# Performance work log

Measured on AMD Instinct MI355X. Metric: run time of the kernel, lower is better.

Reference implementation:

```python
import jax, jax.numpy as jnp
import numpy as np

B, C, H, W = 2, 64, 270, 480
CQ = C // 8


def _distance_weight(n):
    i = jnp.arange(n, dtype=jnp.float32)
    d = i[None, :] - i[:, None]  # j - i
    return jnp.exp(-(d * d) / (2.0 * (n * n / 4.0)))  # [n, n]


def setup_inputs() -> dict:
    key = jax.random.key(0)
    ks = jax.random.split(key, 8)
    s = 0.05
    return {
        "x": jax.random.normal(ks[0], (B, C, H, W), jnp.float32),
        "Wq": jax.random.normal(ks[1], (CQ, C), jnp.float32) * s,
        "bq": jax.random.normal(ks[2], (CQ,), jnp.float32) * s,
        "Wk": jax.random.normal(ks[3], (CQ, C), jnp.float32) * s,
        "bk": jax.random.normal(ks[4], (CQ,), jnp.float32) * s,
        "Wv": jax.random.normal(ks[5], (C, C), jnp.float32) * s,
        "bv": jax.random.normal(ks[6], (C,), jnp.float32) * s,
        "gamma": jax.random.normal(ks[7], (), jnp.float32) * 0.3,
        "dw_h": _distance_weight(H),  # [H, H] non-trainable buffer
        "dw_w": _distance_weight(W),  # [W, W] non-trainable buffer
    }


def reference(x, Wq, bq, Wk, bk, Wv, bv, gamma, dw_h, dw_w):
    # 1x1 convs == per-pixel linear projections
    q = jnp.einsum('oc,bchw->bohw', Wq, x) + bq[None, :, None, None]  # [B,CQ,H,W]
    k = jnp.einsum('oc,bchw->bohw', Wk, x) + bk[None, :, None, None]  # [B,CQ,H,W]
    v = jnp.einsum('oc,bchw->bohw', Wv, x) + bv[None, :, None, None]  # [B,C,H,W]

    height, width = x.shape[2], x.shape[3]
    neg_inf = jnp.float32(-jnp.inf)

    # row (H-direction) energy: queries/keys along the height axis per column w
    e_h = jnp.einsum('bchw,bcgw->bwhg', q, k) * dw_h[None, None]  # [B,W,H,H]
    # diagonal -inf mask (dw_h diag == 1, so order of mul is immaterial)
    eye_h = jnp.eye(height, dtype=bool)
    e_h = jnp.where(eye_h[None, None], neg_inf, e_h)
    e_h = jnp.transpose(e_h, (0, 2, 1, 3))  # [B,H,W,H]

    # column (W-direction) energy along the width axis per row h
    e_w = jnp.einsum('bchw,bchv->bhwv', q, k) * dw_w[None, None]  # [B,H,W,W]

    # joint softmax over concatenated H and W directions
    att = jax.nn.softmax(jnp.concatenate([e_h, e_w], axis=3), axis=3)  # [B,H,W,H+W]
    att_h = jnp.transpose(att[:, :, :, :height], (0, 2, 1, 3))  # [B,W,H,H]
    att_w = att[:, :, :, height:]  # [B,H,W,W]

    out_h = jnp.einsum('bcgw,bwhg->bchw', v, att_h)  # [B,C,H,W]
    out_w = jnp.einsum('bchv,bhwv->bchw', v, att_w)  # [B,C,H,W]

    return gamma * (out_h + out_w) + x
```

## Files before the change

### kernel.cpp

```cpp
#include <hip/hip_runtime.h>
#include <hip/hip_bf16.h>

namespace {

constexpr int B  = 2;
constexpr int C  = 64;
constexpr int CQ = 8;
constexpr int H  = 270;
constexpr int W  = 480;
constexpr int HW = H * W;
constexpr float INVH2 = 2.0f / (270.0f * 270.0f);
constexpr float INVW2 = 2.0f / (480.0f * 480.0f);

typedef __attribute__((ext_vector_type(4))) float f32x4;
typedef __attribute__((ext_vector_type(8))) short short8;
typedef __attribute__((ext_vector_type(4))) unsigned int uint4v;

__device__ __forceinline__ float bits2f(unsigned short u) {
  union { unsigned int i; float f; } cv;
  cv.i = ((unsigned int)u) << 16;
  return cv.f;
}

__device__ __forceinline__ unsigned short f2bf(float f) {
  union { __hip_bfloat16 b; unsigned short u; } cv;
  cv.b = __float2bfloat16(f);
  return cv.u;
}

__device__ __forceinline__ unsigned int pack2(float a, float b) {
  return ((unsigned int)f2bf(b) << 16) | (unsigned int)f2bf(a);
}

__device__ __forceinline__ short8 pack_p(const float p0[4], const float p1[4]) {
  uint4v pw;
  pw[0] = pack2(p0[0], p0[1]);
  pw[1] = pack2(p0[2], p0[3]);
  pw[2] = pack2(p1[0], p1[1]);
  pw[3] = pack2(p1[2], p1[3]);
  return __builtin_bit_cast(short8, pw);
}


__global__ __launch_bounds__(256)
void k_qkv(const float* __restrict__ x,
           const float* __restrict__ Wq, const float* __restrict__ bq,
           const float* __restrict__ Wk, const float* __restrict__ bk,
           const float* __restrict__ Wv, const float* __restrict__ bv,
           unsigned short* __restrict__ qwp, unsigned short* __restrict__ kwp,
           unsigned short* __restrict__ qhp, unsigned short* __restrict__ khp,
           unsigned short* __restrict__ v, unsigned short* __restrict__ vt) {
  __shared__ __align__(16) float wql[CQ * C];
  __shared__ __align__(16) float wkl[CQ * C];
  __shared__ __align__(16) float wvl[C * C];
  __shared__ float bql[CQ], bkl[CQ], bvl[C];
  const int tid = threadIdx.x;
  for (int i = tid; i < CQ * C; i += 256) { wql[i] = Wq[i]; wkl[i] = Wk[i]; }
  for (int i = tid; i < C * C; i += 256) wvl[i] = Wv[i];
  if (tid < CQ) { bql[tid] = bq[tid]; bkl[tid] = bk[tid]; }
  if (tid < C) bvl[tid] = bv[tid];
  __syncthreads();
  const int pix = blockIdx.x * 256 + tid;
  if (pix >= B * HW) return;
  const int b = pix / HW;
  const int r = pix - b * HW;
  const int h = r / W;
  const int w = r - h * W;

  float qa[CQ], ka[CQ], va[C];
#pragma unroll
  for (int o = 0; o < CQ; ++o) { qa[o] = bql[o]; ka[o] = bkl[o]; }
#pragma unroll
  for (int o = 0; o < C; ++o) va[o] = bvl[o];

  const float* xp = x + (size_t)b * C * HW + r;
  for (int c = 0; c < C; c += 4) {
    const float x0 = xp[(size_t)(c + 0) * HW];
    const float x1 = xp[(size_t)(c + 1) * HW];
    const float x2 = xp[(size_t)(c + 2) * HW];
    const float x3 = xp[(size_t)(c + 3) * HW];
#pragma unroll
    for (int o = 0; o < CQ; ++o) {
      const float4 a = *(const float4*)(wql + o * C + c);
      qa[o] = fmaf(a.w, x3, fmaf(a.z, x2, fmaf(a.y, x1, fmaf(a.x, x0, qa[o]))));
      const float4 bb = *(const float4*)(wkl + o * C + c);
      ka[o] = fmaf(bb.w, x3, fmaf(bb.z, x2, fmaf(bb.y, x1, fmaf(bb.x, x0, ka[o]))));
    }
#pragma unroll
    for (int o = 0; o < C; ++o) {
      const float4 cc = *(const float4*)(wvl + o * C + c);
      va[o] = fmaf(cc.w, x3, fmaf(cc.z, x2, fmaf(cc.y, x1, fmaf(cc.x, x0, va[o]))));
    }
  }

  uint4 qp4, kp4;
  qp4.x = pack2(qa[0], qa[1]); qp4.y = pack2(qa[2], qa[3]);
  qp4.z = pack2(qa[4], qa[5]); qp4.w = pack2(qa[6], qa[7]);
  kp4.x = pack2(ka[0], ka[1]); kp4.y = pack2(ka[2], ka[3]);
  kp4.z = pack2(ka[4], ka[5]); kp4.w = pack2(ka[6], ka[7]);
  *(uint4*)(qwp + (size_t)pix * 8) = qp4;
  *(uint4*)(kwp + (size_t)pix * 8) = kp4;
  const size_t tbase = ((size_t)b * W + w) * H + h;
  *(uint4*)(qhp + tbase * 8) = qp4;
  *(uint4*)(khp + tbase * 8) = kp4;

  unsigned short* vp = v + (size_t)b * C * HW + r;
#pragma unroll
  for (int o = 0; o < C; ++o) vp[(size_t)o * HW] = f2bf(va[o]);
  unsigned short* vtp = vt + tbase * C;
#pragma unroll
  for (int j = 0; j < 16; ++j) {
    ushort4 u;
    u.x = f2bf(va[4 * j + 0]);
    u.y = f2bf(va[4 * j + 1]);
    u.z = f2bf(va[4 * j + 2]);
    u.w = f2bf(va[4 * j + 3]);
    *(ushort4*)(vtp + 4 * j) = u;
  }
}

constexpr int VSW = 488;

__global__ __launch_bounds__(960, 1)
void k_outw(const unsigned short* __restrict__ qwp,
            const unsigned short* __restrict__ kwp,
            const unsigned short* __restrict__ v,
            unsigned short* __restrict__ ow, float* __restrict__ Sw) {
  __shared__ __align__(16) unsigned short vbs[31232];
  __shared__ __align__(16) unsigned short kls[480 * 8];
  const int h = blockIdx.x, b = blockIdx.y;
  const int tid = threadIdx.x;
  const size_t rowbase = ((size_t)b * H + h) * W;

  const unsigned short* vrow = v + (size_t)b * C * HW + (size_t)h * W;
  for (int idx = tid; idx < 64 * 120; idx += 960) {
    const int c = idx / 120, s4 = (idx - c * 120) * 4;
    const int u = s4 & 31;
    const int t = (u < 16) ? ((u >> 2) * 8) : (((u - 16) >> 2) * 8 + 4);
    *(ushort4*)(vbs + c * VSW + (s4 & ~31) + t) =
        *(const ushort4*)(vrow + (size_t)c * HW + s4);
  }
  for (int g = tid; g < 480; g += 960)
    *(uint4*)(kls + g * 8) = *(const uint4*)(kwp + (rowbase + g) * 8);

  const int lane = tid & 63, wv = tid >> 6;
  const int l15 = lane & 15, quad = lane >> 4;
  const int m0 = wv * 32;

  short8 qa0 = short8{0, 0, 0, 0, 0, 0, 0, 0};
  short8 qa1 = short8{0, 0, 0, 0, 0, 0, 0, 0};
  if (quad == 0) {
    qa0 = *(const short8*)(qwp + (rowbase + m0 + l15) * 8);
    qa1 = *(const short8*)(qwp + (rowbase + m0 + 16 + l15) * 8);
  }

  f32x4 acc[2][4];
  float Sacc[2] = {0.0f, 0.0f};
#pragma unroll
  for (int mt = 0; mt < 2; ++mt)
#pragma unroll
    for (int ct = 0; ct < 4; ++ct)
#pragma unroll
      for (int rr = 0; rr < 4; ++rr) acc[mt][ct][rr] = 0.0f;

  __syncthreads();

  for (int ci = 0; ci < 15; ++ci) {
    const int sc = ci * 32;
    short8 kb0 = short8{0, 0, 0, 0, 0, 0, 0, 0};
    short8 kb1 = short8{0, 0, 0, 0, 0, 0, 0, 0};
    if (quad == 0) {
      kb0 = *(const short8*)(kls + (sc + l15) * 8);
      kb1 = *(const short8*)(kls + (sc + 16 + l15) * 8);
    }
    const f32x4 z4 = f32x4{0.f, 0.f, 0.f, 0.f};
    const f32x4 E00 = __builtin_amdgcn_mfma_f32_16x16x32_bf16(kb0, qa0, z4, 0, 0, 0);
    const f32x4 E01 = __builtin_amdgcn_mfma_f32_16x16x32_bf16(kb1, qa0, z4, 0, 0, 0);
    const f32x4 E10 = __builtin_amdgcn_mfma_f32_16x16x32_bf16(kb0, qa1, z4, 0, 0, 0);
    const f32x4 E11 = __builtin_amdgcn_mfma_f32_16x16x32_bf16(kb1, qa1, z4, 0, 0, 0);
    short8 vb[4];
#pragma unroll
    for (int ct = 0; ct < 4; ++ct)
      vb[ct] = *(const short8*)(vbs + (ct * 16 + l15) * VSW + sc + quad * 8);
#pragma unroll
    for (int mt = 0; mt < 2; ++mt) {
      const int m = m0 + mt * 16 + l15;
      const f32x4 Ea = mt ? E10 : E00;
      const f32x4 Eb = mt ? E11 : E01;
      float p0[4], p1[4];
#pragma unroll
      for (int rr = 0; rr < 4; ++rr) {
        const float d0 = (float)(m - (sc + quad * 4 + rr));
        const float d1 = d0 - 16.0f;
        p0[rr] = __expf(Ea[rr] * __expf(-(d0 * d0) * INVW2));
        p1[rr] = __expf(Eb[rr] * __expf(-(d1 * d1) * INVW2));
        Sacc[mt] += p0[rr] + p1[rr];
      }
      const short8 pa = pack_p(p0, p1);
#pragma unroll
      for (int ct = 0; ct < 4; ++ct)
        acc[mt][ct] = __builtin_amdgcn_mfma_f32_16x16x32_bf16(pa, vb[ct], acc[mt][ct], 0, 0, 0);
    }
  }

#pragma unroll
  for (int mt = 0; mt < 2; ++mt) {
    float s = Sacc[mt];
    s += __shfl_xor(s, 16);
    s += __shfl_xor(s, 32);
    if (lane < 16) Sw[rowbase + m0 + mt * 16 + l15] = s;
  }

  __syncthreads();
  unsigned short* ob = vbs;
#pragma unroll
  for (int mt = 0; mt < 2; ++mt)
#pragma unroll
    for (int ct = 0; ct < 4; ++ct)
#pragma unroll
      for (int rr = 0; rr < 4; ++rr)
        ob[(ct * 16 + l15) * VSW + m0 + mt * 16 + quad * 4 + rr] = f2bf(acc[mt][ct][rr]);
  __syncthreads();
  unsigned short* og = ow + ((size_t)b * H + h) * C * W;
  for (int idx = tid; idx < 64 * 240; idx += 960) {
    const int c = idx / 240, wp = idx - c * 240;
    *(unsigned int*)(og + (size_t)c * W + 2 * wp) =
        *(const unsigned int*)(ob + c * VSW + 2 * wp);
  }
}

constexpr int VSH = 296;

__global__ __launch_bounds__(576, 1)
void k_outh(const unsigned short* __restrict__ qhp,
            const unsigned short* __restrict__ khp,
            const unsigned short* __restrict__ vt,
            unsigned short* __restrict__ oht, float* __restrict__ Sht) {
  __shared__ __align__(16) unsigned short vbs[18944];
  __shared__ __align__(16) unsigned short kls[288 * 8];
  const int w = blockIdx.x, b = blockIdx.y;
  const int tid = threadIdx.x;
  const size_t colbase = ((size_t)b * W + w) * H;

  const unsigned short* vtb = vt + ((size_t)b * W + w) * H * C;
  for (int idx = tid; idx < 288 * 16; idx += 576) {
    const int g = idx >> 4, c4 = (idx & 15) * 4;
    ushort4 vv = make_ushort4(0, 0, 0, 0);
    if (g < H) vv = *(const ushort4*)(vtb + (size_t)g * C + c4);
    const int u = g & 31;
    const int t = (u < 16) ? ((u >> 2) * 8 + (u & 3))
                           : (((u - 16) >> 2) * 8 + 4 + (u & 3));
    const int slot = (g & ~31) + t;
    vbs[(c4 + 0) * VSH + slot] = vv.x;
    vbs[(c4 + 1) * VSH + slot] = vv.y;
    vbs[(c4 + 2) * VSH + slot] = vv.z;
    vbs[(c4 + 3) * VSH + slot] = vv.w;
  }
  for (int g = tid; g < 288; g += 576)
    *(uint4*)(kls + g * 8) =
        *(const uint4*)(khp + (colbase + min(g, H - 1)) * 8);

  const int lane = tid & 63, wv = tid >> 6;
  const int l15 = lane & 15, quad = lane >> 4;
  const int m0 = wv * 32;

  short8 qa0 = short8{0, 0, 0, 0, 0, 0, 0, 0};
  short8 qa1 = short8{0, 0, 0, 0, 0, 0, 0, 0};
  if (quad == 0) {
    qa0 = *(const short8*)(qhp + (colbase + min(m0 + l15, H - 1)) * 8);
    qa1 = *(const short8*)(qhp + (colbase + min(m0 + 16 + l15, H - 1)) * 8);
  }

  f32x4 acc[2][4];
  float Sacc[2] = {0.0f, 0.0f};
#pragma unroll
  for (int mt = 0; mt < 2; ++mt)
#pragma unroll
    for (int ct = 0; ct < 4; ++ct)
#pragma unroll
      for (int rr = 0; rr < 4; ++rr) acc[mt][ct][rr] = 0.0f;

  __syncthreads();

  for (int ci = 0; ci < 9; ++ci) {
    const int gc = ci * 32;
    short8 kb0 = short8{0, 0, 0, 0, 0, 0, 0, 0};
    short8 kb1 = short8{0, 0, 0, 0, 0, 0, 0, 0};
    if (quad == 0) {
      kb0 = *(const short8*)(kls + (gc + l15) * 8);
      kb1 = *(const short8*)(kls + (gc + 16 + l15) * 8);
    }
    const f32x4 z4 = f32x4{0.f, 0.f, 0.f, 0.f};
    const f32x4 E00 = __builtin_amdgcn_mfma_f32_16x16x32_bf16(kb0, qa0, z4, 0, 0, 0);
    const f32x4 E01 = __builtin_amdgcn_mfma_f32_16x16x32_bf16(kb1, qa0, z4, 0, 0, 0);
    const f32x4 E10 = __builtin_amdgcn_mfma_f32_16x16x32_bf16(kb0, qa1, z4, 0, 0, 0);
    const f32x4 E11 = __builtin_amdgcn_mfma_f32_16x16x32_bf16(kb1, qa1, z4, 0, 0, 0);
    short8 vb[4];
#pragma unroll
    for (int ct = 0; ct < 4; ++ct)
      vb[ct] = *(const short8*)(vbs + (ct * 16 + l15) * VSH + gc + quad * 8);
#pragma unroll
    for (int mt = 0; mt < 2; ++mt) {
      const int m = m0 + mt * 16 + l15;
      const f32x4 Ea = mt ? E10 : E00;
      const f32x4 Eb = mt ? E11 : E01;
      float p0[4], p1[4];
#pragma unroll
      for (int rr = 0; rr < 4; ++rr) {
        const int g0 = gc + quad * 4 + rr;
        const int g1 = g0 + 16;
        const float d0 = (float)(m - g0);
        const float d1 = d0 - 16.0f;
        p0[rr] = (g0 < H && g0 != m)
                     ? __expf(Ea[rr] * __expf(-(d0 * d0) * INVH2)) : 0.0f;
        p1[rr] = (g1 < H && g1 != m)
                     ? __expf(Eb[rr] * __expf(-(d1 * d1) * INVH2)) : 0.0f;
        Sacc[mt] += p0[rr] + p1[rr];
      }
      const short8 pa = pack_p(p0, p1);
#pragma unroll
      for (int ct = 0; ct < 4; ++ct)
        acc[mt][ct] = __builtin_amdgcn_mfma_f32_16x16x32_bf16(pa, vb[ct], acc[mt][ct], 0, 0, 0);
    }
  }

#pragma unroll
  for (int mt = 0; mt < 2; ++mt) {
    float s = Sacc[mt];
    s += __shfl_xor(s, 16);
    s += __shfl_xor(s, 32);
    const int m = m0 + mt * 16 + l15;
    if (lane < 16 && m < H) Sht[colbase + m] = s;
  }

  __syncthreads();
  unsigned short* ob = vbs;
#pragma unroll
  for (int mt = 0; mt < 2; ++mt)
#pragma unroll
    for (int ct = 0; ct < 4; ++ct)
#pragma unroll
      for (int rr = 0; rr < 4; ++rr)
        ob[(ct * 16 + l15) * VSH + m0 + mt * 16 + quad * 4 + rr] = f2bf(acc[mt][ct][rr]);
  __syncthreads();
  unsigned short* og = oht + ((size_t)b * W + w) * C * H;
  for (int idx = tid; idx < 64 * 135; idx += 576) {
    const int c = idx / 135, hp = idx - c * 135;
    *(unsigned int*)(og + (size_t)c * H + 2 * hp) =
        *(const unsigned int*)(ob + c * VSH + 2 * hp);
  }
}

__global__ __launch_bounds__(256)
void k_combine(const unsigned short* __restrict__ oht,
               const unsigned short* __restrict__ ow,
               const float* __restrict__ Sht, const float* __restrict__ Sw,
               const float* __restrict__ x,
               const float* __restrict__ gp,
               float* __restrict__ out) {
  __shared__ float tile[32][33];
  const int b = blockIdx.z >> 6, c = blockIdx.z & 63;
  const int w0 = blockIdx.x * 32, h0 = blockIdx.y * 32;
  const int tx = threadIdx.x, ty = threadIdx.y;
#pragma unroll
  for (int i = 0; i < 4; ++i) {
    const int wl = ty + i * 8;
    const int hh = h0 + tx;
    float val = 0.0f;
    if (hh < H) val = bits2f(oht[(((size_t)b * W + (w0 + wl)) * C + c) * H + hh]);
    tile[wl][tx] = val;
  }
  __syncthreads();
  const float gamma = *gp;
#pragma unroll
  for (int i = 0; i < 4; ++i) {
    const int hl = ty + i * 8;
    const int hh = h0 + hl;
    if (hh < H) {
      const int ww = w0 + tx;
      const float uh = tile[tx][hl];
      const float uw = bits2f(ow[(((size_t)b * H + hh) * C + c) * W + ww]);
      const size_t si = ((size_t)b * H + hh) * W + ww;
      const float Z = Sht[((size_t)b * W + ww) * H + hh] + Sw[si];
      const float invZ = __builtin_amdgcn_rcpf(Z);
      const size_t xi = ((size_t)b * C + c) * HW + (size_t)hh * W + ww;
      out[xi] = fmaf(gamma * invZ, uh + uw, x[xi]);
    }
  }
}

}

extern "C" void kernel_launch(void* const* d_in, const int* in_sizes, int n_in,
                              void* d_out, int out_size, void* d_ws, size_t ws_size,
                              hipStream_t stream) {
  (void)in_sizes; (void)n_in; (void)out_size; (void)ws_size;
  const float* x  = (const float*)d_in[0];
  const float* Wq = (const float*)d_in[1];
  const float* bq = (const float*)d_in[2];
  const float* Wk = (const float*)d_in[3];
  const float* bk = (const float*)d_in[4];
  const float* Wv = (const float*)d_in[5];
  const float* bv = (const float*)d_in[6];
  const float* gp = (const float*)d_in[7];
  float* out = (float*)d_out;

  char* p = (char*)d_ws;
  auto take = [&](size_t bytes) -> void* {
    char* r = p;
    p += (bytes + 255) & ~(size_t)255;
    return (void*)r;
  };
  unsigned short* qwp = (unsigned short*)take(sizeof(unsigned short) * (size_t)B * HW * 8);
  unsigned short* kwp = (unsigned short*)take(sizeof(unsigned short) * (size_t)B * HW * 8);
  unsigned short* qhp = (unsigned short*)take(sizeof(unsigned short) * (size_t)B * HW * 8);
  unsigned short* khp = (unsigned short*)take(sizeof(unsigned short) * (size_t)B * HW * 8);
  unsigned short* v   = (unsigned short*)take(sizeof(unsigned short) * (size_t)B * C * HW);
  unsigned short* vt  = (unsigned short*)take(sizeof(unsigned short) * (size_t)B * C * HW);
  unsigned short* oht = (unsigned short*)take(sizeof(unsigned short) * (size_t)B * C * HW);
  unsigned short* owb = (unsigned short*)take(sizeof(unsigned short) * (size_t)B * C * HW);
  float* Sht = (float*)take(sizeof(float) * (size_t)B * HW);
  float* Sw  = (float*)take(sizeof(float) * (size_t)B * HW);

  hipLaunchKernelGGL(k_qkv, dim3((B * HW + 255) / 256), dim3(256), 0, stream,
                     x, Wq, bq, Wk, bk, Wv, bv, qwp, kwp, qhp, khp, v, vt);
  hipLaunchKernelGGL(k_outh, dim3(W, B), dim3(576), 0, stream,
                     qhp, khp, vt, oht, Sht);
  hipLaunchKernelGGL(k_outw, dim3(H, B), dim3(960), 0, stream,
                     qwp, kwp, v, owb, Sw);
  hipLaunchKernelGGL(k_combine, dim3(W / 32, (H + 31) / 32, B * C), dim3(32, 8), 0, stream,
                     oht, owb, Sht, Sw, x, gp, out);
}
```

Measured before the change: 454.1 us.

## Split row and column attention blocks in two along the query axis

Each k_outw and k_outh block now handles only half of the query chunks, with twice as many smaller blocks (512 and 320 threads). Both halves still stage the full V row or column and K into LDS, and each writes back only its own part of the output. The LDS row strides are also padded differently (494 and 302). The aim is better load balance and more blocks per CU, which may help latency hiding. The cost is that the V/K staging loads are duplicated, and some waves sit idle because 15 and 9 chunks do not split evenly.

```diff
diff --git a/kernel.cpp b/kernel.cpp
--- a/kernel.cpp
+++ b/kernel.cpp
@@ -119,37 +119,40 @@
   }
 }
 
-constexpr int VSW = 488;
-
-__global__ __launch_bounds__(960, 1)
+constexpr int VSW = 494;
+
+__global__ __launch_bounds__(512, 1)
 void k_outw(const unsigned short* __restrict__ qwp,
             const unsigned short* __restrict__ kwp,
             const unsigned short* __restrict__ v,
             unsigned short* __restrict__ ow, float* __restrict__ Sw) {
-  __shared__ __align__(16) unsigned short vbs[31232];
+  __shared__ __align__(16) unsigned short vbs[64 * VSW];
   __shared__ __align__(16) unsigned short kls[480 * 8];
-  const int h = blockIdx.x, b = blockIdx.y;
+  const int h = blockIdx.x >> 1, z = blockIdx.x & 1;
+  const int b = blockIdx.y;
   const int tid = threadIdx.x;
   const size_t rowbase = ((size_t)b * H + h) * W;
 
   const unsigned short* vrow = v + (size_t)b * C * HW + (size_t)h * W;
-  for (int idx = tid; idx < 64 * 120; idx += 960) {
+  for (int idx = tid; idx < 64 * 120; idx += 512) {
     const int c = idx / 120, s4 = (idx - c * 120) * 4;
     const int u = s4 & 31;
     const int t = (u < 16) ? ((u >> 2) * 8) : (((u - 16) >> 2) * 8 + 4);
     *(ushort4*)(vbs + c * VSW + (s4 & ~31) + t) =
         *(const ushort4*)(vrow + (size_t)c * HW + s4);
   }
-  for (int g = tid; g < 480; g += 960)
+  for (int g = tid; g < 480; g += 512)
     *(uint4*)(kls + g * 8) = *(const uint4*)(kwp + (rowbase + g) * 8);
 
   const int lane = tid & 63, wv = tid >> 6;
   const int l15 = lane & 15, quad = lane >> 4;
-  const int m0 = wv * 32;
+  const int chunk = z * 8 + wv;
+  const bool active = chunk < 15;
+  const int m0 = chunk * 32;
 
   short8 qa0 = short8{0, 0, 0, 0, 0, 0, 0, 0};
   short8 qa1 = short8{0, 0, 0, 0, 0, 0, 0, 0};
-  if (quad == 0) {
+  if (quad == 0 && active) {
     qa0 = *(const short8*)(qwp + (rowbase + m0 + l15) * 8);
     qa1 = *(const short8*)(qwp + (rowbase + m0 + 16 + l15) * 8);
   }
@@ -165,85 +168,92 @@
 
   __syncthreads();
 
-  for (int ci = 0; ci < 15; ++ci) {
-    const int sc = ci * 32;
-    short8 kb0 = short8{0, 0, 0, 0, 0, 0, 0, 0};
-    short8 kb1 = short8{0, 0, 0, 0, 0, 0, 0, 0};
-    if (quad == 0) {
-      kb0 = *(const short8*)(kls + (sc + l15) * 8);
-      kb1 = *(const short8*)(kls + (sc + 16 + l15) * 8);
-    }
-    const f32x4 z4 = f32x4{0.f, 0.f, 0.f, 0.f};
-    const f32x4 E00 = __builtin_amdgcn_mfma_f32_16x16x32_bf16(kb0, qa0, z4, 0, 0, 0);
-    const f32x4 E01 = __builtin_amdgcn_mfma_f32_16x16x32_bf16(kb1, qa0, z4, 0, 0, 0);
-    const f32x4 E10 = __builtin_amdgcn_mfma_f32_16x16x32_bf16(kb0, qa1, z4, 0, 0, 0);
-    const f32x4 E11 = __builtin_amdgcn_mfma_f32_16x16x32_bf16(kb1, qa1, z4, 0, 0, 0);
-    short8 vb[4];
-#pragma unroll
-    for (int ct = 0; ct < 4; ++ct)
-      vb[ct] = *(const short8*)(vbs + (ct * 16 + l15) * VSW + sc + quad * 8);
+  if (active) {
+    for (int ci = 0; ci < 15; ++ci) {
+      const int sc = ci * 32;
+      short8 kb0 = short8{0, 0, 0, 0, 0, 0, 0, 0};
+      short8 kb1 = short8{0, 0, 0, 0, 0, 0, 0, 0};
+      if (quad == 0) {
+        kb0 = *(const short8*)(kls + (sc + l15) * 8);
+        kb1 = *(const short8*)(kls + (sc + 16 + l15) * 8);
+      }
+      const f32x4 z4 = f32x4{0.f, 0.f, 0.f, 0.f};
+      const f32x4 E00 = __builtin_amdgcn_mfma_f32_16x16x32_bf16(kb0, qa0, z4, 0, 0, 0);
+      const f32x4 E01 = __builtin_amdgcn_mfma_f32_16x16x32_bf16(kb1, qa0, z4, 0, 0, 0);
+      const f32x4 E10 = __builtin_amdgcn_mfma_f32_16x16x32_bf16(kb0, qa1, z4, 0, 0, 0);
+      const f32x4 E11 = __builtin_amdgcn_mfma_f32_16x16x32_bf16(kb1, qa1, z4, 0, 0, 0);
+      short8 vb[4];
+#pragma unroll
+      for (int ct = 0; ct < 4; ++ct)
+        vb[ct] = *(const short8*)(vbs + (ct * 16 + l15) * VSW + sc + quad * 8);
+#pragma unroll
+      for (int mt = 0; mt < 2; ++mt) {
+        const int m = m0 + mt * 16 + l15;
+        const f32x4 Ea = mt ? E10 : E00;
+        const f32x4 Eb = mt ? E11 : E01;
+        float p0[4], p1[4];
+#pragma unroll
+        for (int rr = 0; rr < 4; ++rr) {
+          const float d0 = (float)(m - (sc + quad * 4 + rr));
+          const float d1 = d0 - 16.0f;
+          p0[rr] = __expf(Ea[rr] * __expf(-(d0 * d0) * INVW2));
+          p1[rr] = __expf(Eb[rr] * __expf(-(d1 * d1) * INVW2));
+          Sacc[mt] += p0[rr] + p1[rr];
+        }
+        const short8 pa = pack_p(p0, p1);
+#pragma unroll
+        for (int ct = 0; ct < 4; ++ct)
+          acc[mt][ct] = __builtin_amdgcn_mfma_f32_16x16x32_bf16(pa, vb[ct], acc[mt][ct], 0, 0, 0);
+      }
+    }
+
 #pragma unroll
     for (int mt = 0; mt < 2; ++mt) {
-      const int m = m0 + mt * 16 + l15;
-      const f32x4 Ea = mt ? E10 : E00;
-      const f32x4 Eb = mt ? E11 : E01;
-      float p0[4], p1[4];
-#pragma unroll
-      for (int rr = 0; rr < 4; ++rr) {
-        const float d0 = (float)(m - (sc + quad * 4 + rr));
-        const float d1 = d0 - 16.0f;
-        p0[rr] = __expf(Ea[rr] * __expf(-(d0 * d0) * INVW2));
-        p1[rr] = __expf(Eb[rr] * __expf(-(d1 * d1) * INVW2));
-        Sacc[mt] += p0[rr] + p1[rr];
-      }
-      const short8 pa = pack_p(p0, p1);
+      float s = Sacc[mt];
+      s += __shfl_xor(s, 16);
+      s += __shfl_xor(s, 32);
+      if (lane < 16) Sw[rowbase + m0 + mt * 16 + l15] = s;
+    }
+  }
+
+  __syncthreads();
+  unsigned short* ob = vbs;
+  if (active) {
+#pragma unroll
+    for (int mt = 0; mt < 2; ++mt)
 #pragma unroll
       for (int ct = 0; ct < 4; ++ct)
-        acc[mt][ct] = __builtin_amdgcn_mfma_f32_16x16x32_bf16(pa, vb[ct], acc[mt][ct], 0, 0, 0);
-    }
-  }
-
-#pragma unroll
-  for (int mt = 0; mt < 2; ++mt) {
-    float s = Sacc[mt];
-    s += __shfl_xor(s, 16);
-    s += __shfl_xor(s, 32);
-    if (lane < 16) Sw[rowbase + m0 + mt * 16 + l15] = s;
-  }
-
-  __syncthreads();
-  unsigned short* ob = vbs;
-#pragma unroll
-  for (int mt = 0; mt < 2; ++mt)
-#pragma unroll
-    for (int ct = 0; ct < 4; ++ct)
-#pragma unroll
-      for (int rr = 0; rr < 4; ++rr)
-        ob[(ct * 16 + l15) * VSW + m0 + mt * 16 + quad * 4 + rr] = f2bf(acc[mt][ct][rr]);
+#pragma unroll
+        for (int rr = 0; rr < 4; ++rr)
+          ob[(ct * 16 + l15) * VSW + m0 + mt * 16 + quad * 4 + rr] = f2bf(acc[mt][ct][rr]);
+  }
   __syncthreads();
   unsigned short* og = ow + ((size_t)b * H + h) * C * W;
-  for (int idx = tid; idx < 64 * 240; idx += 960) {
-    const int c = idx / 240, wp = idx - c * 240;
-    *(unsigned int*)(og + (size_t)c * W + 2 * wp) =
-        *(const unsigned int*)(ob + c * VSW + 2 * wp);
-  }
-}
-
-constexpr int VSH = 296;
-
-__global__ __launch_bounds__(576, 1)
+  const int mlo = z ? 256 : 0;
+  const int nu = z ? 112 : 128;
+  for (int idx = tid; idx < 64 * nu; idx += 512) {
+    const int c = idx / nu, i = idx - c * nu;
+    *(unsigned int*)(og + (size_t)c * W + mlo + 2 * i) =
+        *(const unsigned int*)(ob + c * VSW + mlo + 2 * i);
+  }
+}
+
+constexpr int VSH = 302;
+
+__global__ __launch_bounds__(320, 1)
 void k_outh(const unsigned short* __restrict__ qhp,
             const unsigned short* __restrict__ khp,
             const unsigned short* __restrict__ vt,
             unsigned short* __restrict__ oht, float* __restrict__ Sht) {
-  __shared__ __align__(16) unsigned short vbs[18944];
+  __shared__ __align__(16) unsigned short vbs[64 * VSH];
   __shared__ __align__(16) unsigned short kls[288 * 8];
-  const int w = blockIdx.x, b = blockIdx.y;
+  const int w = blockIdx.x >> 1, z = blockIdx.x & 1;
+  const int b = blockIdx.y;
   const int tid = threadIdx.x;
   const size_t colbase = ((size_t)b * W + w) * H;
 
-  const unsigned short* vtb = vt + ((size_t)b * W + w) * H * C;
-  for (int idx = tid; idx < 288 * 16; idx += 576) {
+  const unsigned short* vtb = vt + colbase * C;
+  for (int idx = tid; idx < 288 * 16; idx += 320) {
     const int g = idx >> 4, c4 = (idx & 15) * 4;
     ushort4 vv = make_ushort4(0, 0, 0, 0);
     if (g < H) vv = *(const ushort4*)(vtb + (size_t)g * C + c4);
@@ -256,17 +266,19 @@
     vbs[(c4 + 2) * VSH + slot] = vv.z;
     vbs[(c4 + 3) * VSH + slot] = vv.w;
   }
-  for (int g = tid; g < 288; g += 576)
+  for (int g = tid; g < 288; g += 320)
     *(uint4*)(kls + g * 8) =
         *(const uint4*)(khp + (colbase + min(g, H - 1)) * 8);
 
   const int lane = tid & 63, wv = tid >> 6;
   const int l15 = lane & 15, quad = lane >> 4;
-  const int m0 = wv * 32;
+  const int chunk = z * 5 + wv;
+  const bool active = chunk < 9;
+  const int m0 = chunk * 32;
 
   short8 qa0 = short8{0, 0, 0, 0, 0, 0, 0, 0};
   short8 qa1 = short8{0, 0, 0, 0, 0, 0, 0, 0};
-  if (quad == 0) {
+  if (quad == 0 && active) {
     qa0 = *(const short8*)(qhp + (colbase + min(m0 + l15, H - 1)) * 8);
     qa1 = *(const short8*)(qhp + (colbase + min(m0 + 16 + l15, H - 1)) * 8);
   }
@@ -282,72 +294,78 @@
 
   __syncthreads();
 
-  for (int ci = 0; ci < 9; ++ci) {
-    const int gc = ci * 32;
-    short8 kb0 = short8{0, 0, 0, 0, 0, 0, 0, 0};
-    short8 kb1 = short8{0, 0, 0, 0, 0, 0, 0, 0};
-    if (quad == 0) {
-      kb0 = *(const short8*)(kls + (gc + l15) * 8);
-      kb1 = *(const short8*)(kls + (gc + 16 + l15) * 8);
-    }
-    const f32x4 z4 = f32x4{0.f, 0.f, 0.f, 0.f};
-    const f32x4 E00 = __builtin_amdgcn_mfma_f32_16x16x32_bf16(kb0, qa0, z4, 0, 0, 0);
-    const f32x4 E01 = __builtin_amdgcn_mfma_f32_16x16x32_bf16(kb1, qa0, z4, 0, 0, 0);
-    const f32x4 E10 = __builtin_amdgcn_mfma_f32_16x16x32_bf16(kb0, qa1, z4, 0, 0, 0);
-    const f32x4 E11 = __builtin_amdgcn_mfma_f32_16x16x32_bf16(kb1, qa1, z4, 0, 0, 0);
-    short8 vb[4];
-#pragma unroll
-    for (int ct = 0; ct < 4; ++ct)
-      vb[ct] = *(const short8*)(vbs + (ct * 16 + l15) * VSH + gc + quad * 8);
+  if (active) {
+    for (int ci = 0; ci < 9; ++ci) {
+      const int gc = ci * 32;
+      short8 kb0 = short8{0, 0, 0, 0, 0, 0, 0, 0};
+      short8 kb1 = short8{0, 0, 0, 0, 0, 0, 0, 0};
+      if (quad == 0) {
+        kb0 = *(const short8*)(kls + (gc + l15) * 8);
+        kb1 = *(const short8*)(kls + (gc + 16 + l15) * 8);
+      }
+      const f32x4 z4 = f32x4{0.f, 0.f, 0.f, 0.f};
+      const f32x4 E00 = __builtin_amdgcn_mfma_f32_16x16x32_bf16(kb0, qa0, z4, 0, 0, 0);
+      const f32x4 E01 = __builtin_amdgcn_mfma_f32_16x16x32_bf16(kb1, qa0, z4, 0, 0, 0);
+      const f32x4 E10 = __builtin_amdgcn_mfma_f32_16x16x32_bf16(kb0, qa1, z4, 0, 0, 0);
+      const f32x4 E11 = __builtin_amdgcn_mfma_f32_16x16x32_bf16(kb1, qa1, z4, 0, 0, 0);
+      short8 vb[4];
+#pragma unroll
+      for (int ct = 0; ct < 4; ++ct)
+        vb[ct] = *(const short8*)(vbs + (ct * 16 + l15) * VSH + gc + quad * 8);
+#pragma unroll
+      for (int mt = 0; mt < 2; ++mt) {
+        const int m = m0 + mt * 16 + l15;
+        const f32x4 Ea = mt ? E10 : E00;
+        const f32x4 Eb = mt ? E11 : E01;
+        float p0[4], p1[4];
+#pragma unroll
+        for (int rr = 0; rr < 4; ++rr) {
+          const int g0 = gc + quad * 4 + rr;
+          const int g1 = g0 + 16;
+          const float d0 = (float)(m - g0);
+          const float d1 = d0 - 16.0f;
+          p0[rr] = (g0 < H && g0 != m)
+                       ? __expf(Ea[rr] * __expf(-(d0 * d0) * INVH2)) : 0.0f;
+          p1[rr] = (g1 < H && g1 != m)
+                       ? __expf(Eb[rr] * __expf(-(d1 * d1) * INVH2)) : 0.0f;
+          Sacc[mt] += p0[rr] + p1[rr];
+        }
+        const short8 pa = pack_p(p0, p1);
+#pragma unroll
+        for (int ct = 0; ct < 4; ++ct)
+          acc[mt][ct] = __builtin_amdgcn_mfma_f32_16x16x32_bf16(pa, vb[ct], acc[mt][ct], 0, 0, 0);
+      }
+    }
+
 #pragma unroll
     for (int mt = 0; mt < 2; ++mt) {
+      float s = Sacc[mt];
+      s += __shfl_xor(s, 16);
+      s += __shfl_xor(s, 32);
       const int m = m0 + mt * 16 + l15;
-      const f32x4 Ea = mt ? E10 : E00;
-      const f32x4 Eb = mt ? E11 : E01;
-      float p0[4], p1[4];
-#pragma unroll
-      for (int rr = 0; rr < 4; ++rr) {
-        const int g0 = gc + quad * 4 + rr;
-        const int g1 = g0 + 16;
-        const float d0 = (float)(m - g0);
-        const float d1 = d0 - 16.0f;
-        p0[rr] = (g0 < H && g0 != m)
-                     ? __expf(Ea[rr] * __expf(-(d0 * d0) * INVH2)) : 0.0f;
-        p1[rr] = (g1 < H && g1 != m)
-                     ? __expf(Eb[rr] * __expf(-(d1 * d1) * INVH2)) : 0.0f;
-        Sacc[mt] += p0[rr] + p1[rr];
-      }
-      const short8 pa = pack_p(p0, p1);
+      if (lane < 16 && m < H) Sht[colbase + m] = s;
+    }
+  }
+
+  __syncthreads();
+  unsigned short* ob = vbs;
+  if (active) {
+#pragma unroll
+    for (int mt = 0; mt < 2; ++mt)
 #pragma unroll
       for (int ct = 0; ct < 4; ++ct)
-        acc[mt][ct] = __builtin_amdgcn_mfma_f32_16x16x32_bf16(pa, vb[ct], acc[mt][ct], 0, 0, 0);
-    }
-  }
-
-#pragma unroll
-  for (int mt = 0; mt < 2; ++mt) {
-    float s = Sacc[mt];
-    s += __shfl_xor(s, 16);
-    s += __shfl_xor(s, 32);
-    const int m = m0 + mt * 16 + l15;
-    if (lane < 16 && m < H) Sht[colbase + m] = s;
-  }
-
-  __syncthreads();
-  unsigned short* ob = vbs;
-#pragma unroll
-  for (int mt = 0; mt < 2; ++mt)
-#pragma unroll
-    for (int ct = 0; ct < 4; ++ct)
-#pragma unroll
-      for (int rr = 0; rr < 4; ++rr)
-        ob[(ct * 16 + l15) * VSH + m0 + mt * 16 + quad * 4 + rr] = f2bf(acc[mt][ct][rr]);
+#pragma unroll
+        for (int rr = 0; rr < 4; ++rr)
+          ob[(ct * 16 + l15) * VSH + m0 + mt * 16 + quad * 4 + rr] = f2bf(acc[mt][ct][rr]);
+  }
   __syncthreads();
   unsigned short* og = oht + ((size_t)b * W + w) * C * H;
-  for (int idx = tid; idx < 64 * 135; idx += 576) {
-    const int c = idx / 135, hp = idx - c * 135;
-    *(unsigned int*)(og + (size_t)c * H + 2 * hp) =
-        *(const unsigned int*)(ob + c * VSH + 2 * hp);
+  const int mlo = z ? 160 : 0;
+  const int nu = z ? 55 : 80;
+  for (int idx = tid; idx < 64 * nu; idx += 320) {
+    const int c = idx / nu, i = idx - c * nu;
+    *(unsigned int*)(og + (size_t)c * H + mlo + 2 * i) =
+        *(const unsigned int*)(ob + c * VSH + mlo + 2 * i);
   }
 }
 
@@ -424,9 +442,9 @@
 
   hipLaunchKernelGGL(k_qkv, dim3((B * HW + 255) / 256), dim3(256), 0, stream,
                      x, Wq, bq, Wk, bk, Wv, bv, qwp, kwp, qhp, khp, v, vt);
-  hipLaunchKernelGGL(k_outh, dim3(W, B), dim3(576), 0, stream,
+  hipLaunchKernelGGL(k_outh, dim3(2 * W, B), dim3(320), 0, stream,
                      qhp, khp, vt, oht, Sht);
-  hipLaunchKernelGGL(k_outw, dim3(H, B), dim3(960), 0, stream,
+  hipLaunchKernelGGL(k_outw, dim3(2 * H, B), dim3(512), 0, stream,
                      qwp, kwp, v, owb, Sw);
   hipLaunchKernelGGL(k_combine, dim3(W / 32, (H + 31) / 32, B * C), dim3(32, 8), 0, stream,
                      oht, owb, Sht, Sw, x, gp, out);
```

After: 445.8 us. About the same (-1.8%).
